# Performance work log

Measured on AMD Instinct MI355X. Metric: run time of the kernel, lower is better.

## Reference

```python
import jax, jax.numpy as jnp
import numpy as np

NEG_SLOPE = 0.2   # RGATConv default negative_slope
BN_EPS = 1e-5     # torch BatchNorm1d default eps


def _build_edges(n0, n1, batch):
    """Replicates generate_edges_union + PyG Batch offsetting. Returns [2, B*E] src/dst and [B*E] edge types."""
    n = n0 + n1
    def perm(k, off):  # itertools.permutations(range(k), 2) as (src, dst) columns
        a = np.repeat(np.arange(k), k); b = np.tile(np.arange(k), k)
        m = a != b
        return np.stack([a[m], b[m]]) + off
    intra = np.concatenate([perm(n0, 0), perm(n1, n0)], axis=1)                 # edge_type 0
    ca = np.repeat(np.arange(n0), n1); cb = np.tile(np.arange(n0, n), n0)
    cross = np.concatenate([np.stack([ca, cb]), np.stack([cb, ca])], axis=1)    # edge_type 1
    edges = np.concatenate([intra, cross], axis=1)
    etype = np.concatenate([np.zeros(intra.shape[1], np.int32), np.ones(cross.shape[1], np.int32)])
    offs = (np.arange(batch) * n)[:, None, None]
    edges_b = (edges[None, :, :] + offs).transpose(1, 0, 2).reshape(2, -1)      # per-graph node offsets
    etype_b = np.tile(etype, batch)
    return jnp.asarray(edges_b, jnp.int32), jnp.asarray(etype_b, jnp.int32)


def _segment_softmax(logits, seg, num_seg):
    m = jax.ops.segment_max(logits, seg, num_segments=num_seg)
    m = jnp.where(jnp.isfinite(m), m, 0.0)
    e = jnp.exp(logits - m[seg])
    s = jax.ops.segment_sum(e, seg, num_segments=num_seg)
    return e / (s[seg] + 1e-16)  # PyG softmax eps


def _rgat_layer(x, src, dst, etype, W, q, k, b, num_nodes):
    # PyG RGATConv: heads=1, dim=1, concat=False, additive-self-attention, across-relation softmax, aggr=add
    H = jnp.einsum('nf,rfe->rne', x, W)            # relation-specific transform: [2, BN, F]
    qs = jnp.einsum('rne,e->rn', H, q)             # q-score per node per relation
    ks = jnp.einsum('rne,e->rn', H, k)
    logit = jax.nn.leaky_relu(qs[etype, dst] + ks[etype, src], NEG_SLOPE)  # [E]
    alpha = _segment_softmax(logit, dst, num_nodes)
    msg = alpha[:, None] * H[etype, src]           # [E, F] per-edge messages
    out = jax.ops.segment_sum(msg, dst, num_segments=num_nodes)
    return out + b                                 # heads=1 -> mean over heads is identity; + bias


def setup_inputs() -> dict:
    key = jax.random.key(0)
    ks = jax.random.split(key, 6)
    B, F, N0, N1, L = 4, 256, 128, 128, 3
    s = 0.05
    return {
        'desc0': jax.random.normal(ks[0], (B, F, N0), jnp.float32),
        'desc1': jax.random.normal(ks[1], (B, F, N1), jnp.float32),
        'conv_w': jax.random.normal(ks[2], (L, 2, F, F), jnp.float32) * s,
        'conv_q': jax.random.normal(ks[3], (L, F), jnp.float32) * s,
        'conv_k': jax.random.normal(ks[4], (L, F), jnp.float32) * s,
        'conv_b': jnp.zeros((L, F), jnp.float32),
        'lin_w': jax.random.normal(ks[5], (L, F, 2 * F), jnp.float32) * s,
        'lin_b': jnp.zeros((L, F), jnp.float32),
        'bn_w': jnp.ones((L, F), jnp.float32),
        'bn_b': jnp.zeros((L, F), jnp.float32),
    }


def reference(desc0, desc1, conv_w, conv_q, conv_k, conv_b, lin_w, lin_b, bn_w, bn_b):
    b, f, n0 = desc0.shape
    n1 = desc1.shape[2]
    n = n0 + n1
    # [B, F, N] -> batched node features [B*N, F]
    x = jnp.concatenate([desc0, desc1], axis=2).transpose(0, 2, 1).reshape(b * n, f)
    edges, etype = _build_edges(n0, n1, b)
    src, dst = edges[0], edges[1]
    num_nodes = b * n
    for i in range(conv_w.shape[0]):
        msg1 = jax.nn.relu(_rgat_layer(x, src, dst, etype, conv_w[i], conv_q[i], conv_k[i], conv_b[i], num_nodes))
        msg2 = jnp.concatenate([x, msg1], axis=1) @ lin_w[i].T + lin_b[i]
        mu = msg2.mean(axis=0)
        var = msg2.var(axis=0)  # biased, as torch BatchNorm uses for normalization (training mode)
        msg3 = bn_w[i] * (msg2 - mu) / jnp.sqrt(var + BN_EPS) + bn_b[i]
        x = x + msg3            # edge_pool[i] == 1 -> no knn_graph rebuild
    x = x.reshape(b, n, f).transpose(0, 2, 1)
    return x[:, :, :n0], x[:, :, n0:]
```

## Files before the change

### kernel.cpp

```cpp
#include <hip/hip_runtime.h>
#include <math.h>


typedef __attribute__((ext_vector_type(8))) short short8;
typedef __attribute__((ext_vector_type(4))) float f32x4;
typedef unsigned short u16;
typedef unsigned int   u32;

__device__ __forceinline__ u16 f2bf(float f) {
    union { float f; u32 u; } v; v.f = f;
    u32 r = v.u + 0x7fffu + ((v.u >> 16) & 1u);
    return (u16)(r >> 16);
}
__device__ __forceinline__ short8 ld8(const u16* p) {
    return __builtin_bit_cast(short8, *(const int4*)p);
}

__global__ __launch_bounds__(256) void k_prep(
    const float* __restrict__ d0, const float* __restrict__ d1,
    const float* __restrict__ conv_w, const float* __restrict__ lin_w,
    float* __restrict__ x, u16* __restrict__ xb,
    u16* __restrict__ Wt, u16* __restrict__ lwb, float* __restrict__ gz) {
    const int t = threadIdx.x;
    if (blockIdx.x < 256) {
        __shared__ float Ts[32 * 33];
        const int tt = blockIdx.x;
        const int b = tt >> 6, rem = tt & 63, ft = rem >> 3, nt = rem & 7;
        const float* src = (nt < 4) ? d0 : d1;
        const int nloc = (nt & 3) * 32;
        {
            int fr = t >> 3, c4 = t & 7;
            float4 v = *(const float4*)&src[b * 32768 + (ft * 32 + fr) * 128 + nloc + c4 * 4];
            Ts[fr * 33 + c4 * 4 + 0] = v.x;
            Ts[fr * 33 + c4 * 4 + 1] = v.y;
            Ts[fr * 33 + c4 * 4 + 2] = v.z;
            Ts[fr * 33 + c4 * 4 + 3] = v.w;
        }
        __syncthreads();
        {
            int nr = t >> 3, f4 = t & 7;
            float4 v;
            v.x = Ts[(f4 * 4 + 0) * 33 + nr];
            v.y = Ts[(f4 * 4 + 1) * 33 + nr];
            v.z = Ts[(f4 * 4 + 2) * 33 + nr];
            v.w = Ts[(f4 * 4 + 3) * 33 + nr];
            int node = b * 256 + nt * 32 + nr;
            int idx = node * 256 + ft * 32 + f4 * 4;
            *(float4*)&x[idx] = v;
            ushort4 hb = {f2bf(v.x), f2bf(v.y), f2bf(v.z), f2bf(v.w)};
            *(ushort4*)&xb[idx] = hb;
        }
    } else if (blockIdx.x < 640) {
        __shared__ float Ts[32 * 33];
        const int tt = blockIdx.x - 256;
        const int mat = tt >> 6, rem = tt & 63, et = rem >> 3, ft = rem & 7;
        {
            int fr = t >> 3, c4 = t & 7;
            float4 v = *(const float4*)&conv_w[mat * 65536 + (ft * 32 + fr) * 256 + et * 32 + c4 * 4];
            Ts[fr * 33 + c4 * 4 + 0] = v.x;
            Ts[fr * 33 + c4 * 4 + 1] = v.y;
            Ts[fr * 33 + c4 * 4 + 2] = v.z;
            Ts[fr * 33 + c4 * 4 + 3] = v.w;
        }
        __syncthreads();
        {
            int er = t >> 3, f4 = t & 7;
            ushort4 hb;
            hb.x = f2bf(Ts[(f4 * 4 + 0) * 33 + er]);
            hb.y = f2bf(Ts[(f4 * 4 + 1) * 33 + er]);
            hb.z = f2bf(Ts[(f4 * 4 + 2) * 33 + er]);
            hb.w = f2bf(Ts[(f4 * 4 + 3) * 33 + er]);
            *(ushort4*)&Wt[mat * 65536 + (et * 32 + er) * 256 + ft * 32 + f4 * 4] = hb;
        }
    } else {
        int o4 = (blockIdx.x - 640) * 256 + t;
        float4 v = *(const float4*)&lin_w[o4 * 4];
        ushort4 hb = {f2bf(v.x), f2bf(v.y), f2bf(v.z), f2bf(v.w)};
        *(ushort4*)&lwb[o4 * 4] = hb;
        if (blockIdx.x == 640) {
            #pragma unroll
            for (int j = 0; j < 6; ++j) gz[j * 256 + t] = 0.f;
        }
    }
}

__global__ __launch_bounds__(256, 1) void k_hqk(
    const float* __restrict__ xprev, const float* __restrict__ msg2,
    const float* __restrict__ gsum, const float* __restrict__ gsumsq,
    const float* __restrict__ bw, const float* __restrict__ bb,
    const u16* __restrict__ cwt,
    const float* __restrict__ cq, const float* __restrict__ ck,
    float* __restrict__ xcur, u16* __restrict__ xb, u16* __restrict__ Ht,
    float* __restrict__ qpart, float* __restrict__ kpart, int do_bn) {
    __shared__ __align__(16) u16 Asub[16 * 264];
    __shared__ __align__(16) float sc[256];
    __shared__ __align__(16) float sh[256];
    const int tid = threadIdx.x;
    const int mt = blockIdx.x >> 3, sg = blockIdx.x & 7;
    const int rel = sg >> 2, eg = sg & 3;
    const int m0 = mt * 16;
    const int lane = tid & 63, widx = tid >> 6;
    const int row = lane & 15, kg = lane >> 4;

    if (do_bn) {
        float s1 = gsum[tid], s2 = gsumsq[tid];
        float mu  = s1 * (1.f / 1024.f);
        float var = s2 * (1.f / 1024.f) - mu * mu;
        float scale = bw[tid] * rsqrtf(var + 1e-5f);
        sc[tid] = scale;
        sh[tid] = bb[tid] - mu * scale;
    }
    __syncthreads();
    #pragma unroll
    for (int p = 0; p < 4; ++p) {
        const int r = p * 4 + (tid >> 6);
        const int c0 = (tid & 63) * 4;
        const int idx = (m0 + r) * 256 + c0;
        float4 v = *(const float4*)&xprev[idx];
        if (do_bn) {
            float4 m = *(const float4*)&msg2[idx];
            float4 s4 = *(const float4*)&sc[c0];
            float4 h4 = *(const float4*)&sh[c0];
            v.x += m.x * s4.x + h4.x;
            v.y += m.y * s4.y + h4.y;
            v.z += m.z * s4.z + h4.z;
            v.w += m.w * s4.w + h4.w;
        }
        ushort4 hb = {f2bf(v.x), f2bf(v.y), f2bf(v.z), f2bf(v.w)};
        *(ushort4*)&Asub[r * 264 + c0] = hb;
        if (do_bn && sg == 0) {
            *(float4*)&xcur[idx] = v;
            *(ushort4*)&xb[idx] = hb;
        }
    }
    __syncthreads();

    const int et = eg * 4 + widx, e0 = et * 16;
    const u16* B = cwt + rel * 65536 + (e0 + row) * 256 + kg * 8;
    const u16* Ap = &Asub[row * 264 + kg * 8];
    f32x4 acc = {0.f,0.f,0.f,0.f};
    #pragma unroll
    for (int k0 = 0; k0 < 256; k0 += 32)
        acc = __builtin_amdgcn_mfma_f32_16x16x32_bf16(ld8(Ap + k0), ld8(B + k0), acc, 0, 0, 0);
    ushort4 o0;
    o0.x = f2bf(acc[0]); o0.y = f2bf(acc[1]); o0.z = f2bf(acc[2]); o0.w = f2bf(acc[3]);
    *(ushort4*)(Ht + rel * 262144 + (e0 + row) * 1024 + m0 + kg * 4) = o0;
    float qe = cq[e0 + row], ke = ck[e0 + row];
    float pq[4], pk[4];
    #pragma unroll
    for (int c = 0; c < 4; ++c) { pq[c] = acc[c] * qe; pk[c] = acc[c] * ke; }
    #pragma unroll
    for (int off = 1; off < 16; off <<= 1) {
        #pragma unroll
        for (int c = 0; c < 4; ++c) {
            pq[c] += __shfl_xor(pq[c], off);
            pk[c] += __shfl_xor(pk[c], off);
        }
    }
    if (row == 0) {
        float4 a4 = {pq[0], pq[1], pq[2], pq[3]};
        float4 b4 = {pk[0], pk[1], pk[2], pk[3]};
        *(float4*)&qpart[(rel * 16 + et) * 1024 + m0 + kg * 4] = a4;
        *(float4*)&kpart[(rel * 16 + et) * 1024 + m0 + kg * 4] = b4;
    }
}

__global__ __launch_bounds__(256, 1) void k_attn_lin(
    const float* __restrict__ qpart, const float* __restrict__ kpart,
    const u16* __restrict__ Ht, const float* __restrict__ cb,
    const u16* __restrict__ xb, const u16* __restrict__ lwp,
    const float* __restrict__ lb,
    float* __restrict__ msg2, float* __restrict__ gsum, float* __restrict__ gsumsq) {
    __shared__ __align__(16) u16 Atile[16 * 264];
    __shared__ __align__(16) u16 M1[16 * 264];
    __shared__ float ksl[2][256];
    __shared__ float qsl[2][16];
    __shared__ __align__(16) float T[4][16 * 20];
    const int tid = threadIdx.x;
    const int mt = blockIdx.x >> 2, nq = blockIdx.x & 3;
    const int m0 = mt * 16;
    const int g = mt >> 4, a = (mt >> 3) & 1;
    {
        float k0s = 0.f, k1s = 0.f;
        #pragma unroll
        for (int c = 0; c < 16; ++c) {
            k0s += kpart[c * 1024 + g * 256 + tid];
            k1s += kpart[(16 + c) * 1024 + g * 256 + tid];
        }
        ksl[0][tid] = k0s; ksl[1][tid] = k1s;
    }
    if (tid < 32) {
        int rel = tid >> 4, r = tid & 15;
        float q = 0.f;
        #pragma unroll
        for (int c = 0; c < 16; ++c) q += qpart[(rel * 16 + c) * 1024 + m0 + r];
        qsl[rel][r] = q;
    }
    __syncthreads();
    {
        const int r = tid >> 4, j = tid & 15;
        const int dl = (m0 + r) & 255;
        const int s0 = j * 16;
        const int rel = ((s0 >> 7) == a) ? 0 : 1;
        float qv = qsl[rel][r];
        float l[16], mx = -1e30f;
        #pragma unroll
        for (int i2 = 0; i2 < 16; ++i2) {
            float v = qv + ksl[rel][s0 + i2];
            v = (v >= 0.f) ? v : 0.2f * v;
            if (s0 + i2 == dl) v = -1e30f;
            l[i2] = v; mx = fmaxf(mx, v);
        }
        #pragma unroll
        for (int off = 1; off < 16; off <<= 1) mx = fmaxf(mx, __shfl_xor(mx, off));
        float s = 0.f;
        #pragma unroll
        for (int i2 = 0; i2 < 16; ++i2) { l[i2] = __expf(l[i2] - mx); s += l[i2]; }
        #pragma unroll
        for (int off = 1; off < 16; off <<= 1) s += __shfl_xor(s, off);
        float inv = 1.f / (s + 1e-16f);
        #pragma unroll
        for (int i2 = 0; i2 < 16; i2 += 2) {
            u32 p = (u32)f2bf(l[i2] * inv) | ((u32)f2bf(l[i2 + 1] * inv) << 16);
            *(u32*)&Atile[r * 264 + s0 + i2] = p;
        }
    }
    __syncthreads();
    const int lane = tid & 63, widx = tid >> 6;
    const int row = lane & 15, kg = lane >> 4;
    const u16* Ap = &Atile[row * 264 + kg * 8];
    float* Tw = &T[widx][0];
    #pragma unroll
    for (int c4 = 0; c4 < 4; ++c4) {
        const int e0 = (widx * 4 + c4) * 16;
        f32x4 acc = {0.f,0.f,0.f,0.f};
        #pragma unroll
        for (int k0 = 0; k0 < 256; k0 += 32) {
            const int rel = (((k0 >> 7) & 1) == a) ? 0 : 1;
            const u16* B = Ht + rel * 262144 + (e0 + row) * 1024 + g * 256 + k0 + kg * 8;
            acc = __builtin_amdgcn_mfma_f32_16x16x32_bf16(ld8(Ap + k0), ld8(B), acc, 0, 0, 0);
        }
        float bias = cb[e0 + row];
        #pragma unroll
        for (int c = 0; c < 4; ++c)
            Tw[(kg * 4 + c) * 20 + row] = fmaxf(acc[c] + bias, 0.f);
        float4 v = *(float4*)&Tw[row * 20 + kg * 4];
        u32 lo = (u32)f2bf(v.x) | ((u32)f2bf(v.y) << 16);
        u32 hi = (u32)f2bf(v.z) | ((u32)f2bf(v.w) << 16);
        uint2 ov = {lo, hi};
        *(uint2*)&M1[row * 264 + e0 + kg * 4] = ov;
    }
    __syncthreads();
    const int n0 = (nq * 4 + widx) * 16;
    const u16* A0 = xb + (m0 + row) * 256 + kg * 8;
    const u16* A1 = &M1[row * 264 + kg * 8];
    const u16* Bl = lwp + (n0 + row) * 512 + kg * 8;
    f32x4 acc = {0.f,0.f,0.f,0.f};
    #pragma unroll
    for (int k0 = 0; k0 < 512; k0 += 32) {
        short8 av = (k0 < 256) ? ld8(A0 + k0) : ld8(A1 + (k0 - 256));
        acc = __builtin_amdgcn_mfma_f32_16x16x32_bf16(av, ld8(Bl + k0), acc, 0, 0, 0);
    }
    float bias = lb[n0 + row];
    float v0 = acc[0] + bias, v1 = acc[1] + bias, v2 = acc[2] + bias, v3 = acc[3] + bias;
    float s1 = v0 + v1 + v2 + v3;
    float s2 = v0 * v0 + v1 * v1 + v2 * v2 + v3 * v3;
    s1 += __shfl_xor(s1, 16); s1 += __shfl_xor(s1, 32);
    s2 += __shfl_xor(s2, 16); s2 += __shfl_xor(s2, 32);
    if (lane < 16) {
        atomicAdd(&gsum[n0 + lane], s1);
        atomicAdd(&gsumsq[n0 + lane], s2);
    }
    Tw[(kg * 4 + 0) * 20 + row] = v0;
    Tw[(kg * 4 + 1) * 20 + row] = v1;
    Tw[(kg * 4 + 2) * 20 + row] = v2;
    Tw[(kg * 4 + 3) * 20 + row] = v3;
    float4 vv = *(float4*)&Tw[row * 20 + kg * 4];
    *(float4*)&msg2[(m0 + row) * 256 + n0 + kg * 4] = vv;
}

__global__ __launch_bounds__(256) void k_fin(
    const float* __restrict__ x2, const float* __restrict__ msg2,
    const float* __restrict__ gsum, const float* __restrict__ gsumsq,
    const float* __restrict__ bw, const float* __restrict__ bb,
    float* __restrict__ out) {
    __shared__ float Tt[32 * 33];
    __shared__ float scf[32];
    __shared__ float shf[32];
    const int t = threadIdx.x;
    const int nt2 = blockIdx.x >> 3, ft = blockIdx.x & 7;
    const int n0 = nt2 * 32, f0 = ft * 32;
    if (t < 32) {
        float s1 = gsum[f0 + t], s2 = gsumsq[f0 + t];
        float mu  = s1 * (1.f / 1024.f);
        float var = s2 * (1.f / 1024.f) - mu * mu;
        float scale = bw[f0 + t] * rsqrtf(var + 1e-5f);
        scf[t] = scale;
        shf[t] = bb[f0 + t] - mu * scale;
    }
    __syncthreads();
    {
        const int nr = t >> 3, f4 = t & 7;
        const int idx = (n0 + nr) * 256 + f0 + f4 * 4;
        float4 v = *(const float4*)&x2[idx];
        float4 m = *(const float4*)&msg2[idx];
        v.x += m.x * scf[f4 * 4 + 0] + shf[f4 * 4 + 0];
        v.y += m.y * scf[f4 * 4 + 1] + shf[f4 * 4 + 1];
        v.z += m.z * scf[f4 * 4 + 2] + shf[f4 * 4 + 2];
        v.w += m.w * scf[f4 * 4 + 3] + shf[f4 * 4 + 3];
        Tt[(f4 * 4 + 0) * 33 + nr] = v.x;
        Tt[(f4 * 4 + 1) * 33 + nr] = v.y;
        Tt[(f4 * 4 + 2) * 33 + nr] = v.z;
        Tt[(f4 * 4 + 3) * 33 + nr] = v.w;
    }
    __syncthreads();
    {
        const int fr = t >> 3, n4 = t & 7;
        const int b = n0 >> 8, half = (n0 >> 7) & 1, nloc = n0 & 127;
        float4 v;
        v.x = Tt[fr * 33 + n4 * 4 + 0];
        v.y = Tt[fr * 33 + n4 * 4 + 1];
        v.z = Tt[fr * 33 + n4 * 4 + 2];
        v.w = Tt[fr * 33 + n4 * 4 + 3];
        *(float4*)&out[half * 131072 + b * 32768 + (f0 + fr) * 128 + nloc + n4 * 4] = v;
    }
}

extern "C" void kernel_launch(void* const* d_in, const int* in_sizes, int n_in,
                              void* d_out, int out_size, void* d_ws, size_t ws_size,
                              hipStream_t stream) {
    const float* desc0  = (const float*)d_in[0];
    const float* desc1  = (const float*)d_in[1];
    const float* conv_w = (const float*)d_in[2];
    const float* conv_q = (const float*)d_in[3];
    const float* conv_k = (const float*)d_in[4];
    const float* conv_b = (const float*)d_in[5];
    const float* lin_w  = (const float*)d_in[6];
    const float* lin_b  = (const float*)d_in[7];
    const float* bn_w   = (const float*)d_in[8];
    const float* bn_b   = (const float*)d_in[9];
    float* out = (float*)d_out;

    char* p = (char*)d_ws;
    float* x0     = (float*)p; p += 1048576;
    float* x1     = (float*)p; p += 1048576;
    u16*   xb     = (u16*)p;   p += 524288;
    u16*   Wt     = (u16*)p;   p += 786432;
    u16*   lwb    = (u16*)p;   p += 786432;
    u16*   Ht     = (u16*)p;   p += 1048576;
    float* qpart  = (float*)p; p += 131072;
    float* kpart  = (float*)p; p += 131072;
    float* msg2   = (float*)p; p += 1048576;
    float* gsA    = (float*)p; p += 3072;
    float* gqA    = (float*)p; p += 3072;

    k_prep<<<1024, 256, 0, stream>>>(desc0, desc1, conv_w, lin_w, x0, xb, Wt, lwb, gsA);

    float* xs[4] = {x0, x0, x1, x0};
    for (int i = 0; i < 3; ++i) {
        const u16*   cwt = Wt + i * 131072;
        const u16*   lwp = lwb + i * 131072;
        const float* cq = conv_q + i * 256;
        const float* ck = conv_k + i * 256;
        const float* cb = conv_b + i * 256;
        const float* lb = lin_b + i * 256;
        const float* bwp = bn_w + (i ? (i - 1) * 256 : 0);
        const float* bbp = bn_b + (i ? (i - 1) * 256 : 0);
        const float* gsp = gsA + (i ? (i - 1) * 256 : 0);
        const float* gqp = gqA + (i ? (i - 1) * 256 : 0);

        k_hqk<<<512, 256, 0, stream>>>(xs[i], msg2, gsp, gqp, bwp, bbp,
                                       cwt, cq, ck, xs[i + 1], xb, Ht,
                                       qpart, kpart, i > 0 ? 1 : 0);
        k_attn_lin<<<256, 256, 0, stream>>>(qpart, kpart, Ht, cb, xb, lwp, lb,
                                            msg2, gsA + i * 256, gqA + i * 256);
    }

    k_fin<<<256, 256, 0, stream>>>(xs[3], msg2, gsA + 512, gqA + 512,
                                   bn_w + 512, bn_b + 512, out);
}
```

Baseline: 156.0 us.

## Consolidate per-row-tile work into single 512-thread blocks with in-block q/k reduction

k_hqk now has each 512-thread block compute every output tile for both relations of one 16-row tile. The q/k score partials are reduced in shared memory, so full qs/ks vectors are written instead of 32 partial slices. k_attn_lin likewise handles all four N-quarters of a row tile in one block and reads the reduced scores directly. This cuts redundant A-tile staging, softmax recomputation and partial-sum traffic, but leaves only 64 blocks per launch on a GPU with many more CUs, which leaves much of the chip idle.

```diff
diff --git a/kernel.cpp b/kernel.cpp
--- a/kernel.cpp
+++ b/kernel.cpp
@@ -84,25 +84,26 @@
     }
 }
 
-__global__ __launch_bounds__(256, 1) void k_hqk(
+__global__ __launch_bounds__(512, 1) void k_hqk(
     const float* __restrict__ xprev, const float* __restrict__ msg2,
     const float* __restrict__ gsum, const float* __restrict__ gsumsq,
     const float* __restrict__ bw, const float* __restrict__ bb,
     const u16* __restrict__ cwt,
     const float* __restrict__ cq, const float* __restrict__ ck,
     float* __restrict__ xcur, u16* __restrict__ xb, u16* __restrict__ Ht,
-    float* __restrict__ qpart, float* __restrict__ kpart, int do_bn) {
+    float* __restrict__ qs, float* __restrict__ ks, int do_bn) {
     __shared__ __align__(16) u16 Asub[16 * 264];
     __shared__ __align__(16) float sc[256];
     __shared__ __align__(16) float sh[256];
+    __shared__ float pQ[2][16][16];
+    __shared__ float pK[2][16][16];
     const int tid = threadIdx.x;
-    const int mt = blockIdx.x >> 3, sg = blockIdx.x & 7;
-    const int rel = sg >> 2, eg = sg & 3;
-    const int m0 = mt * 16;
-    const int lane = tid & 63, widx = tid >> 6;
+    const int m0 = blockIdx.x * 16;
+    const int lane = tid & 63, w = tid >> 6;
     const int row = lane & 15, kg = lane >> 4;
-
-    if (do_bn) {
+    const int rel = w >> 2;
+
+    if (do_bn && tid < 256) {
         float s1 = gsum[tid], s2 = gsumsq[tid];
         float mu  = s1 * (1.f / 1024.f);
         float var = s2 * (1.f / 1024.f) - mu * mu;
@@ -112,8 +113,8 @@
     }
     __syncthreads();
     #pragma unroll
-    for (int p = 0; p < 4; ++p) {
-        const int r = p * 4 + (tid >> 6);
+    for (int p = 0; p < 2; ++p) {
+        const int r = p * 8 + (tid >> 6);
         const int c0 = (tid & 63) * 4;
         const int idx = (m0 + r) * 256 + c0;
         float4 v = *(const float4*)&xprev[idx];
@@ -128,45 +129,59 @@
         }
         ushort4 hb = {f2bf(v.x), f2bf(v.y), f2bf(v.z), f2bf(v.w)};
         *(ushort4*)&Asub[r * 264 + c0] = hb;
-        if (do_bn && sg == 0) {
+        if (do_bn) {
             *(float4*)&xcur[idx] = v;
             *(ushort4*)&xb[idx] = hb;
         }
     }
     __syncthreads();
 
-    const int et = eg * 4 + widx, e0 = et * 16;
-    const u16* B = cwt + rel * 65536 + (e0 + row) * 256 + kg * 8;
     const u16* Ap = &Asub[row * 264 + kg * 8];
-    f32x4 acc = {0.f,0.f,0.f,0.f};
     #pragma unroll
-    for (int k0 = 0; k0 < 256; k0 += 32)
-        acc = __builtin_amdgcn_mfma_f32_16x16x32_bf16(ld8(Ap + k0), ld8(B + k0), acc, 0, 0, 0);
-    ushort4 o0;
-    o0.x = f2bf(acc[0]); o0.y = f2bf(acc[1]); o0.z = f2bf(acc[2]); o0.w = f2bf(acc[3]);
-    *(ushort4*)(Ht + rel * 262144 + (e0 + row) * 1024 + m0 + kg * 4) = o0;
-    float qe = cq[e0 + row], ke = ck[e0 + row];
-    float pq[4], pk[4];
-    #pragma unroll
-    for (int c = 0; c < 4; ++c) { pq[c] = acc[c] * qe; pk[c] = acc[c] * ke; }
-    #pragma unroll
-    for (int off = 1; off < 16; off <<= 1) {
-        #pragma unroll
-        for (int c = 0; c < 4; ++c) {
-            pq[c] += __shfl_xor(pq[c], off);
-            pk[c] += __shfl_xor(pk[c], off);
-        }
-    }
-    if (row == 0) {
-        float4 a4 = {pq[0], pq[1], pq[2], pq[3]};
-        float4 b4 = {pk[0], pk[1], pk[2], pk[3]};
-        *(float4*)&qpart[(rel * 16 + et) * 1024 + m0 + kg * 4] = a4;
-        *(float4*)&kpart[(rel * 16 + et) * 1024 + m0 + kg * 4] = b4;
-    }
-}
-
-__global__ __launch_bounds__(256, 1) void k_attn_lin(
-    const float* __restrict__ qpart, const float* __restrict__ kpart,
+    for (int c4 = 0; c4 < 4; ++c4) {
+        const int tIdx = (w & 3) * 4 + c4;
+        const int e0 = tIdx * 16;
+        const u16* B = cwt + rel * 65536 + (e0 + row) * 256 + kg * 8;
+        f32x4 acc = {0.f,0.f,0.f,0.f};
+        #pragma unroll
+        for (int k0 = 0; k0 < 256; k0 += 32)
+            acc = __builtin_amdgcn_mfma_f32_16x16x32_bf16(ld8(Ap + k0), ld8(B + k0), acc, 0, 0, 0);
+        ushort4 o0;
+        o0.x = f2bf(acc[0]); o0.y = f2bf(acc[1]); o0.z = f2bf(acc[2]); o0.w = f2bf(acc[3]);
+        *(ushort4*)(Ht + rel * 262144 + (e0 + row) * 1024 + m0 + kg * 4) = o0;
+        float qe = cq[e0 + row], ke = ck[e0 + row];
+        float pq[4], pk[4];
+        #pragma unroll
+        for (int c = 0; c < 4; ++c) { pq[c] = acc[c] * qe; pk[c] = acc[c] * ke; }
+        #pragma unroll
+        for (int off = 1; off < 16; off <<= 1) {
+            #pragma unroll
+            for (int c = 0; c < 4; ++c) {
+                pq[c] += __shfl_xor(pq[c], off);
+                pk[c] += __shfl_xor(pk[c], off);
+            }
+        }
+        if (row == 0) {
+            #pragma unroll
+            for (int c = 0; c < 4; ++c) {
+                pQ[rel][tIdx][kg * 4 + c] = pq[c];
+                pK[rel][tIdx][kg * 4 + c] = pk[c];
+            }
+        }
+    }
+    __syncthreads();
+    if (tid < 32) {
+        const int rl = tid >> 4, n = tid & 15;
+        float sq = 0.f, sk = 0.f;
+        #pragma unroll
+        for (int t2 = 0; t2 < 16; ++t2) { sq += pQ[rl][t2][n]; sk += pK[rl][t2][n]; }
+        qs[rl * 1024 + m0 + n] = sq;
+        ks[rl * 1024 + m0 + n] = sk;
+    }
+}
+
+__global__ __launch_bounds__(512, 1) void k_attn_lin(
+    const float* __restrict__ qs, const float* __restrict__ ks,
     const u16* __restrict__ Ht, const float* __restrict__ cb,
     const u16* __restrict__ xb, const u16* __restrict__ lwp,
     const float* __restrict__ lb,
@@ -175,64 +190,56 @@
     __shared__ __align__(16) u16 M1[16 * 264];
     __shared__ float ksl[2][256];
     __shared__ float qsl[2][16];
-    __shared__ __align__(16) float T[4][16 * 20];
+    __shared__ __align__(16) float T[8][16 * 20];
     const int tid = threadIdx.x;
-    const int mt = blockIdx.x >> 2, nq = blockIdx.x & 3;
+    const int mt = blockIdx.x;
     const int m0 = mt * 16;
     const int g = mt >> 4, a = (mt >> 3) & 1;
     {
-        float k0s = 0.f, k1s = 0.f;
-        #pragma unroll
-        for (int c = 0; c < 16; ++c) {
-            k0s += kpart[c * 1024 + g * 256 + tid];
-            k1s += kpart[(16 + c) * 1024 + g * 256 + tid];
-        }
-        ksl[0][tid] = k0s; ksl[1][tid] = k1s;
+        const int rl = tid >> 8, ix = tid & 255;
+        ksl[rl][ix] = ks[rl * 1024 + g * 256 + ix];
     }
     if (tid < 32) {
-        int rel = tid >> 4, r = tid & 15;
-        float q = 0.f;
-        #pragma unroll
-        for (int c = 0; c < 16; ++c) q += qpart[(rel * 16 + c) * 1024 + m0 + r];
-        qsl[rel][r] = q;
+        const int rl = tid >> 4, r = tid & 15;
+        qsl[rl][r] = qs[rl * 1024 + m0 + r];
     }
     __syncthreads();
     {
-        const int r = tid >> 4, j = tid & 15;
+        const int r = tid >> 5, j = tid & 31;
         const int dl = (m0 + r) & 255;
-        const int s0 = j * 16;
+        const int s0 = j * 8;
         const int rel = ((s0 >> 7) == a) ? 0 : 1;
         float qv = qsl[rel][r];
-        float l[16], mx = -1e30f;
-        #pragma unroll
-        for (int i2 = 0; i2 < 16; ++i2) {
+        float l[8], mx = -1e30f;
+        #pragma unroll
+        for (int i2 = 0; i2 < 8; ++i2) {
             float v = qv + ksl[rel][s0 + i2];
             v = (v >= 0.f) ? v : 0.2f * v;
             if (s0 + i2 == dl) v = -1e30f;
             l[i2] = v; mx = fmaxf(mx, v);
         }
         #pragma unroll
-        for (int off = 1; off < 16; off <<= 1) mx = fmaxf(mx, __shfl_xor(mx, off));
+        for (int off = 1; off < 32; off <<= 1) mx = fmaxf(mx, __shfl_xor(mx, off));
         float s = 0.f;
         #pragma unroll
-        for (int i2 = 0; i2 < 16; ++i2) { l[i2] = __expf(l[i2] - mx); s += l[i2]; }
-        #pragma unroll
-        for (int off = 1; off < 16; off <<= 1) s += __shfl_xor(s, off);
+        for (int i2 = 0; i2 < 8; ++i2) { l[i2] = __expf(l[i2] - mx); s += l[i2]; }
+        #pragma unroll
+        for (int off = 1; off < 32; off <<= 1) s += __shfl_xor(s, off);
         float inv = 1.f / (s + 1e-16f);
         #pragma unroll
-        for (int i2 = 0; i2 < 16; i2 += 2) {
+        for (int i2 = 0; i2 < 8; i2 += 2) {
             u32 p = (u32)f2bf(l[i2] * inv) | ((u32)f2bf(l[i2 + 1] * inv) << 16);
             *(u32*)&Atile[r * 264 + s0 + i2] = p;
         }
     }
     __syncthreads();
-    const int lane = tid & 63, widx = tid >> 6;
+    const int lane = tid & 63, w = tid >> 6;
     const int row = lane & 15, kg = lane >> 4;
     const u16* Ap = &Atile[row * 264 + kg * 8];
-    float* Tw = &T[widx][0];
+    float* Tw = &T[w][0];
     #pragma unroll
-    for (int c4 = 0; c4 < 4; ++c4) {
-        const int e0 = (widx * 4 + c4) * 16;
+    for (int c4 = 0; c4 < 2; ++c4) {
+        const int e0 = (w * 2 + c4) * 16;
         f32x4 acc = {0.f,0.f,0.f,0.f};
         #pragma unroll
         for (int k0 = 0; k0 < 256; k0 += 32) {
@@ -251,32 +258,35 @@
         *(uint2*)&M1[row * 264 + e0 + kg * 4] = ov;
     }
     __syncthreads();
-    const int n0 = (nq * 4 + widx) * 16;
     const u16* A0 = xb + (m0 + row) * 256 + kg * 8;
     const u16* A1 = &M1[row * 264 + kg * 8];
-    const u16* Bl = lwp + (n0 + row) * 512 + kg * 8;
-    f32x4 acc = {0.f,0.f,0.f,0.f};
     #pragma unroll
-    for (int k0 = 0; k0 < 512; k0 += 32) {
-        short8 av = (k0 < 256) ? ld8(A0 + k0) : ld8(A1 + (k0 - 256));
-        acc = __builtin_amdgcn_mfma_f32_16x16x32_bf16(av, ld8(Bl + k0), acc, 0, 0, 0);
-    }
-    float bias = lb[n0 + row];
-    float v0 = acc[0] + bias, v1 = acc[1] + bias, v2 = acc[2] + bias, v3 = acc[3] + bias;
-    float s1 = v0 + v1 + v2 + v3;
-    float s2 = v0 * v0 + v1 * v1 + v2 * v2 + v3 * v3;
-    s1 += __shfl_xor(s1, 16); s1 += __shfl_xor(s1, 32);
-    s2 += __shfl_xor(s2, 16); s2 += __shfl_xor(s2, 32);
-    if (lane < 16) {
-        atomicAdd(&gsum[n0 + lane], s1);
-        atomicAdd(&gsumsq[n0 + lane], s2);
-    }
-    Tw[(kg * 4 + 0) * 20 + row] = v0;
-    Tw[(kg * 4 + 1) * 20 + row] = v1;
-    Tw[(kg * 4 + 2) * 20 + row] = v2;
-    Tw[(kg * 4 + 3) * 20 + row] = v3;
-    float4 vv = *(float4*)&Tw[row * 20 + kg * 4];
-    *(float4*)&msg2[(m0 + row) * 256 + n0 + kg * 4] = vv;
+    for (int c4 = 0; c4 < 2; ++c4) {
+        const int n0 = (w * 2 + c4) * 16;
+        const u16* Bl = lwp + (n0 + row) * 512 + kg * 8;
+        f32x4 acc = {0.f,0.f,0.f,0.f};
+        #pragma unroll
+        for (int k0 = 0; k0 < 512; k0 += 32) {
+            short8 av = (k0 < 256) ? ld8(A0 + k0) : ld8(A1 + (k0 - 256));
+            acc = __builtin_amdgcn_mfma_f32_16x16x32_bf16(av, ld8(Bl + k0), acc, 0, 0, 0);
+        }
+        float bias = lb[n0 + row];
+        float v0 = acc[0] + bias, v1 = acc[1] + bias, v2 = acc[2] + bias, v3 = acc[3] + bias;
+        float s1 = v0 + v1 + v2 + v3;
+        float s2 = v0 * v0 + v1 * v1 + v2 * v2 + v3 * v3;
+        s1 += __shfl_xor(s1, 16); s1 += __shfl_xor(s1, 32);
+        s2 += __shfl_xor(s2, 16); s2 += __shfl_xor(s2, 32);
+        if (lane < 16) {
+            atomicAdd(&gsum[n0 + lane], s1);
+            atomicAdd(&gsumsq[n0 + lane], s2);
+        }
+        Tw[(kg * 4 + 0) * 20 + row] = v0;
+        Tw[(kg * 4 + 1) * 20 + row] = v1;
+        Tw[(kg * 4 + 2) * 20 + row] = v2;
+        Tw[(kg * 4 + 3) * 20 + row] = v3;
+        float4 vv = *(float4*)&Tw[row * 20 + kg * 4];
+        *(float4*)&msg2[(m0 + row) * 256 + n0 + kg * 4] = vv;
+    }
 }
 
 __global__ __launch_bounds__(256) void k_fin(
@@ -348,8 +358,8 @@
     u16*   Wt     = (u16*)p;   p += 786432;
     u16*   lwb    = (u16*)p;   p += 786432;
     u16*   Ht     = (u16*)p;   p += 1048576;
-    float* qpart  = (float*)p; p += 131072;
-    float* kpart  = (float*)p; p += 131072;
+    float* qsb    = (float*)p; p += 8192;
+    float* ksb    = (float*)p; p += 8192;
     float* msg2   = (float*)p; p += 1048576;
     float* gsA    = (float*)p; p += 3072;
     float* gqA    = (float*)p; p += 3072;
@@ -369,11 +379,11 @@
         const float* gsp = gsA + (i ? (i - 1) * 256 : 0);
         const float* gqp = gqA + (i ? (i - 1) * 256 : 0);
 
-        k_hqk<<<512, 256, 0, stream>>>(xs[i], msg2, gsp, gqp, bwp, bbp,
-                                       cwt, cq, ck, xs[i + 1], xb, Ht,
-                                       qpart, kpart, i > 0 ? 1 : 0);
-        k_attn_lin<<<256, 256, 0, stream>>>(qpart, kpart, Ht, cb, xb, lwp, lb,
-                                            msg2, gsA + i * 256, gqA + i * 256);
+        k_hqk<<<64, 512, 0, stream>>>(xs[i], msg2, gsp, gqp, bwp, bbp,
+                                      cwt, cq, ck, xs[i + 1], xb, Ht,
+                                      qsb, ksb, i > 0 ? 1 : 0);
+        k_attn_lin<<<64, 512, 0, stream>>>(qsb, ksb, Ht, cb, xb, lwp, lb,
+                                           msg2, gsA + i * 256, gqA + i * 256);
     }
 
     k_fin<<<256, 256, 0, stream>>>(xs[3], msg2, gsA + 512, gqA + 512,
```

Result: slower. 167.6 us (+7.4%).
